# Optimization experiments

Measured on AMD Instinct MI355X. Metric: run time of the kernel, lower is better.

## Reference

```python
import jax, jax.numpy as jnp
import numpy as np

N_HEAD = 16
W_SCALE = 0.02  # keep pre-softmax scores in a sane range


def setup_inputs() -> dict:
    key = jax.random.key(0)
    ks = jax.random.split(key, 9)
    B, T, C = 4, 2048, 1024
    x = jax.random.normal(ks[0], (B, T, C), dtype=jnp.float32)
    def w(k):
        return jax.random.normal(k, (C, C), dtype=jnp.float32) * W_SCALE
    return {
        "x": x,
        "Wq": w(ks[1]), "bq": jnp.zeros((C,), jnp.float32),
        "Wk": w(ks[2]), "bk": jnp.zeros((C,), jnp.float32),
        "Wv": w(ks[3]), "bv": jnp.zeros((C,), jnp.float32),
        "Wp": w(ks[4]), "bp": jnp.zeros((C,), jnp.float32),
    }


def reference(x, Wq, bq, Wk, bk, Wv, bv, Wp, bp):
    # Causal self-attention, prefill path (layer_past=None, use_cache=False),
    # dropout in eval mode (pdrop=0). Weights stored as [in, out]: y = x @ W + b.
    B, T, C = x.shape
    H = N_HEAD
    d = C // H
    # project and split heads: [B, H, T, d]
    def heads(W, b):
        return (jnp.einsum("btc,cd->btd", x, W) + b).reshape(B, T, H, d).transpose(0, 2, 1, 3)
    q = heads(Wq, bq)
    k = heads(Wk, bk)
    v = heads(Wv, bv)
    scale = 1.0 / jnp.sqrt(jnp.asarray(d, x.dtype))
    att = jnp.einsum("bhtd,bhsd->bhts", q, k) * scale  # [B, H, T, T]
    # causal mask: position t attends to s <= t
    causal = jnp.tril(jnp.ones((T, T), dtype=bool))
    att = jnp.where(causal[None, None, :, :], att, jnp.asarray(-jnp.inf, att.dtype))
    att = jax.nn.softmax(att, axis=-1)
    y = jnp.einsum("bhts,bhsd->bhtd", att, v)  # [B, H, T, d]
    y = y.transpose(0, 2, 1, 3).reshape(B, T, C)
    y = jnp.einsum("btc,cd->btd", y, Wp) + bp
    return y
```

## Files before the change

### kernel.cpp

```cpp
#include <hip/hip_runtime.h>

typedef unsigned short u16;
typedef __attribute__((ext_vector_type(8))) short bf16x8;
typedef __attribute__((ext_vector_type(4))) float f32x4;

__device__ __forceinline__ float bf2f(u16 h) {
    return __uint_as_float(((unsigned int)h) << 16);
}
__device__ __forceinline__ u16 f2bf(float f) {
    unsigned int u = __float_as_uint(f);
    u += 0x7FFFu + ((u >> 16) & 1u);
    return (u16)(u >> 16);
}

__device__ __forceinline__ void gl2lds16(const u16* g, u16* l) {
    __builtin_amdgcn_global_load_lds(
        (const __attribute__((address_space(1))) unsigned int*)g,
        (__attribute__((address_space(3))) unsigned int*)l,
        16, 0, 0);
}

__global__ void detect_dtype(const u16* __restrict__ x, int* __restrict__ flag) {
    __shared__ int cnt;
    if (threadIdx.x == 0) cnt = 0;
    __syncthreads();
    unsigned e = (x[2 * threadIdx.x] >> 7) & 0xFF;
    if (e >= 116 && e <= 132) atomicAdd(&cnt, 1);
    __syncthreads();
    if (threadIdx.x == 0) *flag = (cnt >= 96) ? 1 : 0;
}

__global__ __launch_bounds__(256) void convert_in(
    const void* __restrict__ in, u16* __restrict__ out, long n4,
    const int* __restrict__ flag)
{
    long i = (long)blockIdx.x * blockDim.x + threadIdx.x;
    if (i >= n4) return;
    if (*flag) {
        ((ushort4*)out)[i] = ((const ushort4*)in)[i];
    } else {
        float4 v = ((const float4*)in)[i];
        ushort4 r;
        r.x = f2bf(v.x); r.y = f2bf(v.y); r.z = f2bf(v.z); r.w = f2bf(v.w);
        ((ushort4*)out)[i] = r;
    }
}

__global__ __launch_bounds__(256) void transpose_conv(
    const void* __restrict__ in, u16* __restrict__ out, int R, int Cc,
    const int* __restrict__ flag)
{
    __shared__ u16 tile[32][33];
    int tx = threadIdx.x & 31, ty = threadIdx.x >> 5;
    int c0 = blockIdx.x * 32, r0 = blockIdx.y * 32;
    bool isbf = (*flag != 0);
#pragma unroll
    for (int g = 0; g < 4; ++g) {
        size_t idx = (size_t)(r0 + ty + g * 8) * Cc + c0 + tx;
        tile[ty + g * 8][tx] = isbf ? ((const u16*)in)[idx]
                                    : f2bf(((const float*)in)[idx]);
    }
    __syncthreads();
#pragma unroll
    for (int g = 0; g < 4; ++g)
        out[(size_t)(c0 + ty + g * 8) * R + r0 + tx] = tile[tx][ty + g * 8];
}

__global__ __launch_bounds__(256, 2) void gemm_qkv(
    const u16* __restrict__ A, const u16* __restrict__ Bt,
    const void* __restrict__ biasq, const void* __restrict__ biask,
    const void* __restrict__ biasv,
    u16* __restrict__ Qo, u16* __restrict__ Ko, u16* __restrict__ Vt,
    int M, int K, const int* __restrict__ flag)
{
    __shared__ __align__(16) u16 As[128 * 64];
    __shared__ __align__(16) u16 Bs[128 * 64];

    const int tid  = threadIdx.x;
    const int m0   = blockIdx.y * 128, n0 = blockIdx.x * 128;
    const int lane = tid & 63, wid = tid >> 6;
    const int wm   = (wid >> 1) * 64, wn = (wid & 1) * 64;
    const int m16  = lane & 15, quad = lane >> 4;
    const int isbf = *flag;

    const int srow   = wid * 8 + (lane >> 3);
    const int schunk = (lane & 7) * 8;

    f32x4 acc[4][4];
#pragma unroll
    for (int i = 0; i < 4; ++i)
#pragma unroll
        for (int j = 0; j < 4; ++j)
            acc[i][j] = (f32x4){0.f, 0.f, 0.f, 0.f};

    for (int k0 = 0; k0 < K; k0 += 64) {
#pragma unroll
        for (int g = 0; g < 4; ++g) {
            int r = g * 32 + srow;
            gl2lds16(&A[(size_t)(m0 + r) * K + k0 + schunk], &As[r * 64 + schunk]);
            gl2lds16(&Bt[(size_t)(n0 + r) * K + k0 + schunk], &Bs[r * 64 + schunk]);
        }
        __syncthreads();
#pragma unroll
        for (int ks = 0; ks < 64; ks += 32) {
            bf16x8 a[4], b[4];
#pragma unroll
            for (int i = 0; i < 4; ++i)
                a[i] = *(bf16x8*)&As[(wm + i * 16 + m16) * 64 + ks + quad * 8];
#pragma unroll
            for (int j = 0; j < 4; ++j)
                b[j] = *(bf16x8*)&Bs[(wn + j * 16 + m16) * 64 + ks + quad * 8];
#pragma unroll
            for (int i = 0; i < 4; ++i)
#pragma unroll
                for (int j = 0; j < 4; ++j)
                    acc[i][j] = __builtin_amdgcn_mfma_f32_16x16x32_bf16(
                        a[i], b[j], acc[i][j], 0, 0, 0);
        }
        __syncthreads();
    }

    const int region = n0 >> 10;
    const void* bias = (region == 0) ? biasq : (region == 1) ? biask : biasv;
    const int nbase = region << 10;
    const float osc = (region == 0) ? (0.125f * 1.44269504f) : 1.0f;

#pragma unroll
    for (int i = 0; i < 4; ++i) {
        int grow = m0 + wm + i * 16 + quad * 4;
#pragma unroll
        for (int j = 0; j < 4; ++j) {
            int gcol = n0 + wn + j * 16 + m16;
            int nl = gcol - nbase;
            float bv_ = isbf ? bf2f(((const u16*)bias)[nl])
                             : ((const float*)bias)[nl];
            if (region < 2) {
                u16* out = (region == 0) ? Qo : Ko;
#pragma unroll
                for (int r = 0; r < 4; ++r)
                    out[(size_t)(grow + r) * 1024 + nl] =
                        f2bf((acc[i][j][r] + bv_) * osc);
            } else {
                int h = nl >> 6, dd = nl & 63;
                int bb = grow >> 11, s = grow & 2047;
                ushort4 pk;
                pk.x = f2bf(acc[i][j][0] + bv_);
                pk.y = f2bf(acc[i][j][1] + bv_);
                pk.z = f2bf(acc[i][j][2] + bv_);
                pk.w = f2bf(acc[i][j][3] + bv_);
                *(ushort4*)&Vt[(((size_t)bb * 16 + h) * 64 + dd) * 2048 + s] = pk;
            }
        }
    }
}

__global__ __launch_bounds__(256, 2) void gemm_bias(
    const u16* __restrict__ A, const u16* __restrict__ Bt,
    const void* __restrict__ bias, void* __restrict__ C,
    int M, int N, int K, int final_out, const int* __restrict__ flag)
{
    __shared__ __align__(16) u16 As[128 * 64];
    __shared__ __align__(16) u16 Bs[128 * 64];

    const int tid  = threadIdx.x;
    const int m0   = blockIdx.y * 128, n0 = blockIdx.x * 128;
    const int lane = tid & 63, wid = tid >> 6;
    const int wm   = (wid >> 1) * 64, wn = (wid & 1) * 64;
    const int m16  = lane & 15, quad = lane >> 4;
    const int isbf = *flag;

    const int srow   = wid * 8 + (lane >> 3);
    const int schunk = (lane & 7) * 8;

    f32x4 acc[4][4];
#pragma unroll
    for (int i = 0; i < 4; ++i)
#pragma unroll
        for (int j = 0; j < 4; ++j)
            acc[i][j] = (f32x4){0.f, 0.f, 0.f, 0.f};

    for (int k0 = 0; k0 < K; k0 += 64) {
#pragma unroll
        for (int g = 0; g < 4; ++g) {
            int r = g * 32 + srow;
            gl2lds16(&A[(size_t)(m0 + r) * K + k0 + schunk], &As[r * 64 + schunk]);
            gl2lds16(&Bt[(size_t)(n0 + r) * K + k0 + schunk], &Bs[r * 64 + schunk]);
        }
        __syncthreads();
#pragma unroll
        for (int ks = 0; ks < 64; ks += 32) {
            bf16x8 a[4], b[4];
#pragma unroll
            for (int i = 0; i < 4; ++i)
                a[i] = *(bf16x8*)&As[(wm + i * 16 + m16) * 64 + ks + quad * 8];
#pragma unroll
            for (int j = 0; j < 4; ++j)
                b[j] = *(bf16x8*)&Bs[(wn + j * 16 + m16) * 64 + ks + quad * 8];
#pragma unroll
            for (int i = 0; i < 4; ++i)
#pragma unroll
                for (int j = 0; j < 4; ++j)
                    acc[i][j] = __builtin_amdgcn_mfma_f32_16x16x32_bf16(
                        a[i], b[j], acc[i][j], 0, 0, 0);
        }
        __syncthreads();
    }

    const bool out_f32 = final_out && !isbf;
#pragma unroll
    for (int i = 0; i < 4; ++i) {
        int grow = m0 + wm + i * 16 + quad * 4;
#pragma unroll
        for (int j = 0; j < 4; ++j) {
            int gcol = n0 + wn + j * 16 + m16;
            float bv = isbf ? bf2f(((const u16*)bias)[gcol])
                            : ((const float*)bias)[gcol];
#pragma unroll
            for (int r = 0; r < 4; ++r) {
                float val = acc[i][j][r] + bv;
                size_t idx = (size_t)(grow + r) * N + gcol;
                if (out_f32) ((float*)C)[idx] = val;
                else         ((u16*)C)[idx]   = f2bf(val);
            }
        }
    }
}

__global__ __launch_bounds__(256, 2) void attn_flash(
    const u16* __restrict__ Q, const u16* __restrict__ Kb,
    const u16* __restrict__ Vt, u16* __restrict__ O, int T, int C)
{
    __shared__ __align__(16) u16 Ks[2][128 * 64];
    __shared__ __align__(16) u16 Vts[2][64 * 128];
    __shared__ __align__(16) u16 Ps[128 * 64];

    const int tid  = threadIdx.x;
    const int lane = tid & 63, wid = tid >> 6;
    const int m16  = lane & 15, quad = lane >> 4;
    const int sw   = m16 & 7;
    const float NEG = -3.0e4f;

    const int lin = (int)(blockIdx.x +
                          gridDim.x * (blockIdx.y + gridDim.y * blockIdx.z));
    const int bh  = (lin & 7) + 8 * ((lin >> 3) & 7);
    const int bx  = lin >> 6;
    const int b = bh >> 4, h = bh & 15;

    const size_t headoff = ((size_t)b * T) * C + h * 64;
    const size_t vthead  = ((size_t)bh * 64) * T;
    const int ntiles = 16;

    for (int phase = 0; phase < 2; ++phase) {
        const int qt = phase ? bx : (ntiles - 1) - bx;
        if (phase) __syncthreads();

        bf16x8 aq[2][2];
#pragma unroll
        for (int i = 0; i < 2; ++i)
#pragma unroll
            for (int ks = 0; ks < 2; ++ks)
                aq[i][ks] = *(const bf16x8*)&Q[headoff +
                    (size_t)(qt * 128 + wid * 32 + i * 16 + m16) * C +
                    ks * 32 + quad * 8];

#pragma unroll
        for (int g = 0; g < 4; ++g) {
            int r  = g * 32 + wid * 8 + (lane >> 3);
            int cg = (lane & 7) ^ (r & 7);
            gl2lds16(&Kb[headoff + (size_t)r * C + cg * 8],
                     &Ks[0][r * 64 + (lane & 7) * 8]);
        }
#pragma unroll
        for (int g = 0; g < 4; ++g) {
            int r  = g * 16 + wid * 4 + (lane >> 4);
            int cg = (lane & 15) ^ (r & 7);
            gl2lds16(&Vt[vthead + (size_t)r * T + cg * 8],
                     &Vts[0][r * 128 + (lane & 15) * 8]);
        }

        float l_run[2] = {0.f, 0.f};
        f32x4 o_acc[2][4];
#pragma unroll
        for (int i = 0; i < 2; ++i)
#pragma unroll
            for (int n = 0; n < 4; ++n)
                o_acc[i][n] = (f32x4){0.f, 0.f, 0.f, 0.f};

        for (int st = 0; st <= qt; ++st) {
            __syncthreads();
            const int cur = st & 1;

            if (st < qt) {
                const int nxt = cur ^ 1;
#pragma unroll
                for (int g = 0; g < 4; ++g) {
                    int r  = g * 32 + wid * 8 + (lane >> 3);
                    int cg = (lane & 7) ^ (r & 7);
                    gl2lds16(&Kb[headoff + (size_t)((st + 1) * 128 + r) * C + cg * 8],
                             &Ks[nxt][r * 64 + (lane & 7) * 8]);
                }
#pragma unroll
                for (int g = 0; g < 4; ++g) {
                    int r  = g * 16 + wid * 4 + (lane >> 4);
                    int cg = (lane & 15) ^ (r & 7);
                    gl2lds16(&Vt[vthead + (size_t)r * T + (st + 1) * 128 + cg * 8],
                             &Vts[nxt][r * 128 + (lane & 15) * 8]);
                }
            }

            f32x4 sacc[2][8];
#pragma unroll
            for (int i = 0; i < 2; ++i)
#pragma unroll
                for (int j = 0; j < 8; ++j)
                    sacc[i][j] = (f32x4){0.f, 0.f, 0.f, 0.f};
#pragma unroll
            for (int ks = 0; ks < 2; ++ks) {
                bf16x8 bk[8];
#pragma unroll
                for (int j = 0; j < 8; ++j)
                    bk[j] = *(bf16x8*)&Ks[cur][(j * 16 + m16) * 64 +
                                              (((ks * 4 + quad) ^ sw) * 8)];
#pragma unroll
                for (int i = 0; i < 2; ++i)
#pragma unroll
                    for (int j = 0; j < 8; ++j)
                        sacc[i][j] = __builtin_amdgcn_mfma_f32_16x16x32_bf16(
                            bk[j], aq[i][ks], sacc[i][j], 0, 0, 0);
            }

            if (st == qt) {
#pragma unroll
                for (int i = 0; i < 2; ++i) {
                    const int q_in = wid * 32 + i * 16 + m16;
#pragma unroll
                    for (int j = 0; j < 8; ++j)
#pragma unroll
                        for (int r = 0; r < 4; ++r)
                            if ((j * 16 + quad * 4 + r) > q_in)
                                sacc[i][j][r] = NEG;
                }
            }

            float rs[2] = {0.f, 0.f};
#pragma unroll
            for (int half = 0; half < 2; ++half) {
#pragma unroll
                for (int i = 0; i < 2; ++i) {
#pragma unroll
                    for (int jh = 0; jh < 4; ++jh) {
                        int j = half * 4 + jh;
                        float p0 = exp2f(sacc[i][j][0]);
                        float p1 = exp2f(sacc[i][j][1]);
                        float p2 = exp2f(sacc[i][j][2]);
                        float p3 = exp2f(sacc[i][j][3]);
                        rs[i] += (p0 + p1) + (p2 + p3);
                        unsigned lo = ((__float_as_uint(p0) + 0x8000u) >> 16) |
                                      ((__float_as_uint(p1) + 0x8000u) & 0xFFFF0000u);
                        unsigned hi = ((__float_as_uint(p2) + 0x8000u) >> 16) |
                                      ((__float_as_uint(p3) + 0x8000u) & 0xFFFF0000u);
                        *(uint2*)&Ps[(wid * 32 + i * 16 + m16) * 64 +
                                     (((jh * 2 + (quad >> 1)) ^ sw) * 8) +
                                     (quad & 1) * 4] = make_uint2(lo, hi);
                    }
                }
#pragma unroll
                for (int k4l = 0; k4l < 2; ++k4l) {
                    int k4 = half * 2 + k4l;
                    bf16x8 ap[2], bv[4];
#pragma unroll
                    for (int i = 0; i < 2; ++i)
                        ap[i] = *(bf16x8*)&Ps[(wid * 32 + i * 16 + m16) * 64 +
                                              (((k4l * 4 + quad) ^ sw) * 8)];
#pragma unroll
                    for (int n = 0; n < 4; ++n)
                        bv[n] = *(bf16x8*)&Vts[cur][(n * 16 + m16) * 128 +
                                                   (((k4 * 4 + quad) ^ sw) * 8)];
#pragma unroll
                    for (int i = 0; i < 2; ++i)
#pragma unroll
                        for (int n = 0; n < 4; ++n)
                            o_acc[i][n] = __builtin_amdgcn_mfma_f32_16x16x32_bf16(
                                ap[i], bv[n], o_acc[i][n], 0, 0, 0);
                }
            }
            l_run[0] += rs[0];
            l_run[1] += rs[1];
        }

#pragma unroll
        for (int i = 0; i < 2; ++i) {
            l_run[i] += __shfl_xor(l_run[i], 16);
            l_run[i] += __shfl_xor(l_run[i], 32);
            float linv[4];
#pragma unroll
            for (int r = 0; r < 4; ++r)
                linv[r] = 1.f / __shfl(l_run[i], quad * 4 + r);
#pragma unroll
            for (int n = 0; n < 4; ++n) {
#pragma unroll
                for (int r = 0; r < 4; ++r) {
                    int tq = qt * 128 + wid * 32 + i * 16 + quad * 4 + r;
                    O[((size_t)b * T + tq) * C + h * 64 + n * 16 + m16] =
                        f2bf(o_acc[i][n][r] * linv[r]);
                }
            }
        }
    }
}

extern "C" void kernel_launch(void* const* d_in, const int* in_sizes, int n_in,
                              void* d_out, int out_size, void* d_ws, size_t ws_size,
                              hipStream_t stream)
{
    const void* x  = d_in[0];
    const void* Wq = d_in[1];
    const void* bq = d_in[2];
    const void* Wk = d_in[3];
    const void* bk = d_in[4];
    const void* Wv = d_in[5];
    const void* bv = d_in[6];
    const void* Wp = d_in[7];
    const void* bp = d_in[8];

    const int Bb = 4, T = 2048, C = 1024, H = 16;
    const int M = Bb * T, N = C, K = C;

    u16* wsp = (u16*)d_ws;
    const size_t WSZ = (size_t)C * C;
    const size_t MSZ = (size_t)M * C;
    u16* WtQKV = wsp;
    u16* WtP   = wsp + 3 * WSZ;
    u16* xb    = wsp + 4 * WSZ;
    u16* Qb    = xb + MSZ;
    u16* Kbf   = Qb + MSZ;
    u16* Vtb   = Kbf + MSZ;
    u16* tmp   = Vtb + MSZ;
    int* flag  = (int*)(tmp + MSZ);

    detect_dtype<<<1, 128, 0, stream>>>((const u16*)x, flag);
    convert_in<<<(int)(MSZ / 4 / 256), 256, 0, stream>>>(x, xb, MSZ / 4, flag);

    dim3 tb(256), tg(C / 32, C / 32);
    transpose_conv<<<tg, tb, 0, stream>>>(Wq, WtQKV,           C, C, flag);
    transpose_conv<<<tg, tb, 0, stream>>>(Wk, WtQKV + WSZ,     C, C, flag);
    transpose_conv<<<tg, tb, 0, stream>>>(Wv, WtQKV + 2 * WSZ, C, C, flag);
    transpose_conv<<<tg, tb, 0, stream>>>(Wp, WtP,             C, C, flag);

    dim3 qg(3 * N / 128, M / 128), qb(256);
    gemm_qkv<<<qg, qb, 0, stream>>>(xb, WtQKV, bq, bk, bv, Qb, Kbf, Vtb,
                                    M, K, flag);

    dim3 ag(T / 256, H, Bb), ab(256);
    attn_flash<<<ag, ab, 0, stream>>>(Qb, Kbf, Vtb, tmp, T, C);

    dim3 gg(N / 128, M / 128), gb(256);
    gemm_bias<<<gg, gb, 0, stream>>>(tmp, WtP, bp, d_out, M, N, K, 1, flag);
}
```

Before: 285.9 us.

## XOR-swizzle LDS tiles in GEMMs and merge weight transposes into one launch

The global-to-LDS loads in both GEMM kernels now permute 16-byte chunks by XOR with the row index, and the MFMA fragment reads apply the matching XOR. With a 64-element row stride, the old layout made the 16 rows read by a fragment land on the same LDS banks. The four weight transpose launches are merged into one kernel that uses blockIdx.z to select the matrix, which removes three launches. The swizzle adds a little index arithmetic per load.

```diff
diff --git a/kernel.cpp b/kernel.cpp
--- a/kernel.cpp
+++ b/kernel.cpp
@@ -46,13 +46,18 @@
     }
 }
 
-__global__ __launch_bounds__(256) void transpose_conv(
-    const void* __restrict__ in, u16* __restrict__ out, int R, int Cc,
-    const int* __restrict__ flag)
+__global__ __launch_bounds__(256) void transpose_all(
+    const void* __restrict__ W0, const void* __restrict__ W1,
+    const void* __restrict__ W2, const void* __restrict__ W3,
+    u16* __restrict__ outQKV, u16* __restrict__ outP,
+    int Cc, const int* __restrict__ flag)
 {
     __shared__ u16 tile[32][33];
     int tx = threadIdx.x & 31, ty = threadIdx.x >> 5;
     int c0 = blockIdx.x * 32, r0 = blockIdx.y * 32;
+    int z = blockIdx.z;
+    const void* in = (z == 0) ? W0 : (z == 1) ? W1 : (z == 2) ? W2 : W3;
+    u16* out = (z < 3) ? (outQKV + (size_t)z * Cc * Cc) : outP;
     bool isbf = (*flag != 0);
 #pragma unroll
     for (int g = 0; g < 4; ++g) {
@@ -63,7 +68,7 @@
     __syncthreads();
 #pragma unroll
     for (int g = 0; g < 4; ++g)
-        out[(size_t)(c0 + ty + g * 8) * R + r0 + tx] = tile[tx][ty + g * 8];
+        out[(size_t)(c0 + ty + g * 8) * Cc + r0 + tx] = tile[tx][ty + g * 8];
 }
 
 __global__ __launch_bounds__(256, 2) void gemm_qkv(
@@ -81,10 +86,11 @@
     const int lane = tid & 63, wid = tid >> 6;
     const int wm   = (wid >> 1) * 64, wn = (wid & 1) * 64;
     const int m16  = lane & 15, quad = lane >> 4;
+    const int sw   = m16 & 7;
     const int isbf = *flag;
 
-    const int srow   = wid * 8 + (lane >> 3);
-    const int schunk = (lane & 7) * 8;
+    const int srow = wid * 8 + (lane >> 3);
+    const int sch  = lane & 7;
 
     f32x4 acc[4][4];
 #pragma unroll
@@ -96,20 +102,25 @@
     for (int k0 = 0; k0 < K; k0 += 64) {
 #pragma unroll
         for (int g = 0; g < 4; ++g) {
-            int r = g * 32 + srow;
-            gl2lds16(&A[(size_t)(m0 + r) * K + k0 + schunk], &As[r * 64 + schunk]);
-            gl2lds16(&Bt[(size_t)(n0 + r) * K + k0 + schunk], &Bs[r * 64 + schunk]);
+            int r  = g * 32 + srow;
+            int cg = sch ^ (r & 7);
+            gl2lds16(&A[(size_t)(m0 + r) * K + k0 + cg * 8], &As[r * 64 + sch * 8]);
+            gl2lds16(&Bt[(size_t)(n0 + r) * K + k0 + cg * 8], &Bs[r * 64 + sch * 8]);
         }
         __syncthreads();
 #pragma unroll
-        for (int ks = 0; ks < 64; ks += 32) {
+        for (int ks = 0; ks < 2; ++ks) {
             bf16x8 a[4], b[4];
 #pragma unroll
-            for (int i = 0; i < 4; ++i)
-                a[i] = *(bf16x8*)&As[(wm + i * 16 + m16) * 64 + ks + quad * 8];
-#pragma unroll
-            for (int j = 0; j < 4; ++j)
-                b[j] = *(bf16x8*)&Bs[(wn + j * 16 + m16) * 64 + ks + quad * 8];
+            for (int i = 0; i < 4; ++i) {
+                int row = wm + i * 16 + m16;
+                a[i] = *(bf16x8*)&As[row * 64 + (((ks * 4 + quad) ^ sw) * 8)];
+            }
+#pragma unroll
+            for (int j = 0; j < 4; ++j) {
+                int row = wn + j * 16 + m16;
+                b[j] = *(bf16x8*)&Bs[row * 64 + (((ks * 4 + quad) ^ sw) * 8)];
+            }
 #pragma unroll
             for (int i = 0; i < 4; ++i)
 #pragma unroll
@@ -167,10 +178,11 @@
     const int lane = tid & 63, wid = tid >> 6;
     const int wm   = (wid >> 1) * 64, wn = (wid & 1) * 64;
     const int m16  = lane & 15, quad = lane >> 4;
+    const int sw   = m16 & 7;
     const int isbf = *flag;
 
-    const int srow   = wid * 8 + (lane >> 3);
-    const int schunk = (lane & 7) * 8;
+    const int srow = wid * 8 + (lane >> 3);
+    const int sch  = lane & 7;
 
     f32x4 acc[4][4];
 #pragma unroll
@@ -182,20 +194,25 @@
     for (int k0 = 0; k0 < K; k0 += 64) {
 #pragma unroll
         for (int g = 0; g < 4; ++g) {
-            int r = g * 32 + srow;
-            gl2lds16(&A[(size_t)(m0 + r) * K + k0 + schunk], &As[r * 64 + schunk]);
-            gl2lds16(&Bt[(size_t)(n0 + r) * K + k0 + schunk], &Bs[r * 64 + schunk]);
+            int r  = g * 32 + srow;
+            int cg = sch ^ (r & 7);
+            gl2lds16(&A[(size_t)(m0 + r) * K + k0 + cg * 8], &As[r * 64 + sch * 8]);
+            gl2lds16(&Bt[(size_t)(n0 + r) * K + k0 + cg * 8], &Bs[r * 64 + sch * 8]);
         }
         __syncthreads();
 #pragma unroll
-        for (int ks = 0; ks < 64; ks += 32) {
+        for (int ks = 0; ks < 2; ++ks) {
             bf16x8 a[4], b[4];
 #pragma unroll
-            for (int i = 0; i < 4; ++i)
-                a[i] = *(bf16x8*)&As[(wm + i * 16 + m16) * 64 + ks + quad * 8];
-#pragma unroll
-            for (int j = 0; j < 4; ++j)
-                b[j] = *(bf16x8*)&Bs[(wn + j * 16 + m16) * 64 + ks + quad * 8];
+            for (int i = 0; i < 4; ++i) {
+                int row = wm + i * 16 + m16;
+                a[i] = *(bf16x8*)&As[row * 64 + (((ks * 4 + quad) ^ sw) * 8)];
+            }
+#pragma unroll
+            for (int j = 0; j < 4; ++j) {
+                int row = wn + j * 16 + m16;
+                b[j] = *(bf16x8*)&Bs[row * 64 + (((ks * 4 + quad) ^ sw) * 8)];
+            }
 #pragma unroll
             for (int i = 0; i < 4; ++i)
 #pragma unroll
@@ -441,11 +458,8 @@
     detect_dtype<<<1, 128, 0, stream>>>((const u16*)x, flag);
     convert_in<<<(int)(MSZ / 4 / 256), 256, 0, stream>>>(x, xb, MSZ / 4, flag);
 
-    dim3 tb(256), tg(C / 32, C / 32);
-    transpose_conv<<<tg, tb, 0, stream>>>(Wq, WtQKV,           C, C, flag);
-    transpose_conv<<<tg, tb, 0, stream>>>(Wk, WtQKV + WSZ,     C, C, flag);
-    transpose_conv<<<tg, tb, 0, stream>>>(Wv, WtQKV + 2 * WSZ, C, C, flag);
-    transpose_conv<<<tg, tb, 0, stream>>>(Wp, WtP,             C, C, flag);
+    dim3 tg(C / 32, C / 32, 4), tb(256);
+    transpose_all<<<tg, tb, 0, stream>>>(Wq, Wk, Wv, Wp, WtQKV, WtP, C, flag);
 
     dim3 qg(3 * N / 128, M / 128), qb(256);
     gemm_qkv<<<qg, qb, 0, stream>>>(xb, WtQKV, bq, bk, bv, Qb, Kbf, Vtb,
```

Result: no change. 280.9 us (-1.8%).
